# Optimization experiments

Measured on AMD Instinct MI355X. Metric: run time of the kernel, lower is better.

## Reference

```python
import jax, jax.numpy as jnp
import numpy as np

N = 100000      # nodes
E = 1600000     # edges (avg degree 16)
DIN = 128
DH = 128
DOUT = 16
G = 512         # graphs in batch


def setup_inputs() -> dict:
    key = jax.random.key(0)
    ks = jax.random.split(key, 12)
    def lin(k, fan_in, shape):
        return jax.random.uniform(k, shape, jnp.float32, -1.0, 1.0) / np.sqrt(fan_in)
    return {
        "x": jax.random.normal(ks[0], (N, DIN), jnp.float32),
        "edge_index": jax.random.randint(ks[1], (2, E), 0, N, jnp.int32),
        "edge_weight": jax.random.uniform(ks[2], (E,), jnp.float32),
        "batch": jnp.sort(jax.random.randint(ks[3], (N,), 0, G, jnp.int32)),
        "W1": lin(ks[4], DIN, (DIN, DH)), "b1": jnp.zeros((DH,), jnp.float32),
        "W2": lin(ks[5], DH, (DH, DH)),  "b2": jnp.zeros((DH,), jnp.float32),
        "W3": lin(ks[6], DH, (DH, DH)),  "b3": jnp.zeros((DH,), jnp.float32),
        "Wlin": lin(ks[7], DH, (DH, DOUT)), "blin": lin(ks[8], DH, (DOUT,)),
    }


def gcn_norm(edge_index, edge_weight, num_nodes):
    # PyG gcn_norm: add self-loops (weight 1), symmetric normalization
    loop = jnp.arange(num_nodes, dtype=edge_index.dtype)
    row = jnp.concatenate([edge_index[0], loop])
    col = jnp.concatenate([edge_index[1], loop])
    ew = jnp.concatenate([edge_weight, jnp.ones((num_nodes,), edge_weight.dtype)])
    deg = jax.ops.segment_sum(ew, col, num_segments=num_nodes)
    dinv = jnp.where(deg > 0, jax.lax.rsqrt(jnp.where(deg > 0, deg, 1.0)), 0.0)
    norm = dinv[row] * ew * dinv[col]
    return row, col, norm


def gcn_conv(x, W, b, row, col, norm, num_nodes):
    h = x @ W                                   # [N, d_out]
    msg = h[row] * norm[:, None]                # gather + scale  [E+N, d_out]
    out = jax.ops.segment_sum(msg, col, num_segments=num_nodes)
    return out + b


def reference(x, edge_index, edge_weight, batch, W1, b1, W2, b2, W3, b3, Wlin, blin):
    num_nodes = x.shape[0]
    row, col, norm = gcn_norm(edge_index, edge_weight, num_nodes)
    h = jax.nn.relu(gcn_conv(x, W1, b1, row, col, norm, num_nodes))
    h = jax.nn.relu(gcn_conv(h, W2, b2, row, col, norm, num_nodes))
    h = gcn_conv(h, W3, b3, row, col, norm, num_nodes)
    # global mean pool over graphs
    sums = jax.ops.segment_sum(h, batch, num_segments=G)          # [G, DH]
    cnt = jax.ops.segment_sum(jnp.ones((num_nodes,), h.dtype), batch, num_segments=G)
    hG = sums / jnp.maximum(cnt, 1.0)[:, None]
    # dropout is identity in eval mode
    return hG @ Wlin + blin
```

## Files before the change

### kernel.cpp

```cpp
#include <hip/hip_runtime.h>
#include <hip/hip_bf16.h>

#define NB 512
#define MAXBKT 512
#define PB 4

typedef __attribute__((ext_vector_type(8))) unsigned short ushort8;
typedef __attribute__((ext_vector_type(8))) short bf16x8;
typedef __attribute__((ext_vector_type(4))) float f32x4;

__device__ __forceinline__ unsigned short f2bf(float f) {
    unsigned u = __float_as_uint(f);
    unsigned r = (u + 0x7FFF + ((u >> 16) & 1)) >> 16;
    return (unsigned short)r;
}

__global__ __launch_bounds__(256) void k_wt3_hist(const float* __restrict__ W1,
                                                  const float* __restrict__ W2,
                                                  const float* __restrict__ W3,
                                                  const float* __restrict__ Wlin,
                                                  unsigned short* __restrict__ WT1,
                                                  unsigned short* __restrict__ WT2,
                                                  unsigned short* __restrict__ WLT,
                                                  const int* __restrict__ col, int E, int e2,
                                                  int per, int* __restrict__ cnt, int nbkt) {
    int b = blockIdx.x;
    if (b < 128) {
        const float* W = (b < 64) ? W1 : W2;
        unsigned short* WT = (b < 64) ? WT1 : WT2;
        int idx = (b & 63) * 256 + threadIdx.x;
        int nn = idx >> 7, k = idx & 127;
        WT[nn * 128 + k] = f2bf(W[k * 128 + nn]);
        return;
    }
    if (b < 136) {
        int idx = (b - 128) * 256 + threadIdx.x;
        int c = idx >> 7, k = idx & 127;
        float s = 0.f;
        for (int j = 0; j < 128; ++j) s += W3[k * 128 + j] * Wlin[j * 16 + c];
        WLT[c * 128 + k] = f2bf(s);
        return;
    }
    int hb = b - 136;
    __shared__ int h[MAXBKT];
    int t = threadIdx.x;
    for (int i = t; i < nbkt; i += 256) h[i] = 0;
    __syncthreads();
    int s = hb * per, e = min(s + per, e2);
    for (int i = s + t; i < e; i += 256) {
        int dst = (i < E) ? col[i] : i - E;
        atomicAdd(&h[dst >> 8], 1);
    }
    __syncthreads();
    for (int i = t; i < nbkt; i += 256) cnt[i * NB + hb] = h[i];
}

#define SCAN_T 256
#define SCAN_E 1024

__global__ void k_scan_a(const int* __restrict__ cnt, int n,
                         int* __restrict__ outp, int* __restrict__ bsum) {
    __shared__ int s[SCAN_T];
    int t = threadIdx.x, b = blockIdx.x;
    int base = b * SCAN_E + t * 4;
    int c0 = (base + 0 < n) ? cnt[base + 0] : 0;
    int c1 = (base + 1 < n) ? cnt[base + 1] : 0;
    int c2 = (base + 2 < n) ? cnt[base + 2] : 0;
    int c3 = (base + 3 < n) ? cnt[base + 3] : 0;
    int tsum = c0 + c1 + c2 + c3;
    s[t] = tsum; __syncthreads();
    for (int off = 1; off < SCAN_T; off <<= 1) {
        int v = (t >= off) ? s[t - off] : 0;
        __syncthreads();
        s[t] += v;
        __syncthreads();
    }
    int excl = s[t] - tsum;
    if (base + 0 < n) outp[base + 0] = excl;
    if (base + 1 < n) outp[base + 1] = excl + c0;
    if (base + 2 < n) outp[base + 2] = excl + c0 + c1;
    if (base + 3 < n) outp[base + 3] = excl + c0 + c1 + c2;
    if (t == 0) bsum[b] = s[SCAN_T - 1];
}

__global__ __launch_bounds__(256) void k_scan_b(int* __restrict__ bsum, int nb) {
    __shared__ int s[256];
    int t = threadIdx.x;
    int v = (t < nb) ? bsum[t] : 0;
    s[t] = v; __syncthreads();
    for (int off = 1; off < 256; off <<= 1) {
        int u = (t >= off) ? s[t - off] : 0;
        __syncthreads();
        s[t] += u;
        __syncthreads();
    }
    if (t < nb) bsum[t] = s[t] - v;
}

__global__ __launch_bounds__(256) void k_scatter1(const int* __restrict__ row,
                                                  const int* __restrict__ col,
                                                  const float* __restrict__ ew,
                                                  int E, int e2, int per,
                                                  const int* __restrict__ S,
                                                  const int* __restrict__ bsum,
                                                  uint2* __restrict__ csrR, int nbkt) {
    __shared__ int cur[MAXBKT];
    int t = threadIdx.x;
    for (int i = t; i < nbkt; i += 256) {
        int idx = i * NB + blockIdx.x;
        cur[i] = S[idx] + bsum[idx >> 10];
    }
    __syncthreads();
    int s = blockIdx.x * per, e = min(s + per, e2);
    for (int i = s + t; i < e; i += 256) {
        int src, dst; float w;
        if (i < E) { src = row[i]; dst = col[i]; w = ew[i]; }
        else       { src = dst = i - E; w = 1.0f; }
        int slot = atomicAdd(&cur[dst >> 8], 1);
        csrR[slot] = make_uint2(((unsigned)src << 8) | (unsigned)(dst & 255),
                                __float_as_uint(w));
    }
}

__global__ __launch_bounds__(256) void k_build(const uint2* __restrict__ csrR,
                                               const int* __restrict__ S,
                                               const int* __restrict__ bsum,
                                               int n, int e2,
                                               float2* __restrict__ csrF,
                                               float* __restrict__ dinv,
                                               int* __restrict__ rowptr, int nbkt) {
    __shared__ int   cnt[256];
    __shared__ float wsm[256];
    __shared__ int   off[256];
    __shared__ float dvs[256];
    __shared__ int   curs[256];
    int b = blockIdx.x, t = threadIdx.x;
    cnt[t] = 0; wsm[t] = 0.f;
    __syncthreads();
    int i0 = b * NB;
    int base = S[i0] + bsum[i0 >> 10];
    int end;
    if (b + 1 < nbkt) { int i1 = (b + 1) * NB; end = S[i1] + bsum[i1 >> 10]; }
    else end = e2;
    for (int i = base + t; i < end; i += 256) {
        uint2 r = csrR[i];
        int d = r.x & 255;
        atomicAdd(&cnt[d], 1);
        atomicAdd(&wsm[d], __uint_as_float(r.y));
    }
    __syncthreads();
    int   myc = cnt[t];
    float w   = wsm[t];
    float dv  = (w > 0.f) ? rsqrtf(w) : 0.f;
    dvs[t] = dv;
    off[t] = myc;
    __syncthreads();
    for (int o = 1; o < 256; o <<= 1) {
        int v = (t >= o) ? off[t - o] : 0;
        __syncthreads();
        off[t] += v;
        __syncthreads();
    }
    int excl = off[t] - myc;
    int node = b * 256 + t;
    if (node < n) { dinv[node] = dv; rowptr[node] = base + excl; }
    if (b == nbkt - 1 && t == 0) rowptr[n] = e2;
    curs[t] = excl;
    __syncthreads();
    for (int i = base + t; i < end; i += 256) {
        uint2 r = csrR[i];
        int d = r.x & 255;
        int src = (int)(r.x >> 8);
        int p = base + atomicAdd(&curs[d], 1);
        csrF[p] = make_float2(__int_as_float(src), __uint_as_float(r.y) * dvs[d]);
    }
}

template<typename T>
__global__ __launch_bounds__(256) void k_gemm_mfma(const T* __restrict__ H,
                                                   const unsigned short* __restrict__ WT,
                                                   const float* __restrict__ dinv,
                                                   unsigned short* __restrict__ O, int n) {
    int wv = threadIdx.x >> 6, lane = threadIdx.x & 63;
    int rowBase = blockIdx.x * 64 + wv * 16;
    int lr = lane & 15;
    int lk = (lane >> 4) * 8;

    int arow = min(rowBase + lr, n - 1);
    bf16x8 a[4];
#pragma unroll
    for (int kk = 0; kk < 4; ++kk) {
        if constexpr (sizeof(T) == 4) {
            const float4* p = (const float4*)&H[(size_t)arow * 128 + kk * 32 + lk];
            float4 h0 = p[0], h1 = p[1];
            bf16x8 av;
            av[0] = (short)f2bf(h0.x); av[1] = (short)f2bf(h0.y);
            av[2] = (short)f2bf(h0.z); av[3] = (short)f2bf(h0.w);
            av[4] = (short)f2bf(h1.x); av[5] = (short)f2bf(h1.y);
            av[6] = (short)f2bf(h1.z); av[7] = (short)f2bf(h1.w);
            a[kk] = av;
        } else {
            a[kk] = *(const bf16x8*)&H[(size_t)arow * 128 + kk * 32 + lk];
        }
    }

    f32x4 acc[8] = {};
#pragma unroll
    for (int c = 0; c < 8; ++c) {
#pragma unroll
        for (int kk = 0; kk < 4; ++kk) {
            bf16x8 b = *(const bf16x8*)&WT[(size_t)(c * 16 + lr) * 128 + kk * 32 + lk];
            acc[c] = __builtin_amdgcn_mfma_f32_16x16x32_bf16(a[kk], b, acc[c], 0, 0, 0);
        }
    }

#pragma unroll
    for (int r = 0; r < 4; ++r) {
        int node = rowBase + (lane >> 4) * 4 + r;
        if (node < n) {
            float sc = dinv[node];
#pragma unroll
            for (int c = 0; c < 8; ++c)
                O[(size_t)node * 128 + c * 16 + lr] = f2bf(acc[c][r] * sc);
        }
    }
}

__global__ __launch_bounds__(256) void k_gemmP(const unsigned short* __restrict__ H,
                                               const unsigned short* __restrict__ WLT,
                                               const float* __restrict__ dinv,
                                               float* __restrict__ P, int n) {
    int wv = threadIdx.x >> 6, lane = threadIdx.x & 63;
    int rowBase = blockIdx.x * 64 + wv * 16;
    int lr = lane & 15;
    int lk = (lane >> 4) * 8;

    int arow = min(rowBase + lr, n - 1);
    f32x4 acc = {};
#pragma unroll
    for (int kk = 0; kk < 4; ++kk) {
        bf16x8 a = *(const bf16x8*)&H[(size_t)arow * 128 + kk * 32 + lk];
        bf16x8 b = *(const bf16x8*)&WLT[(size_t)lr * 128 + kk * 32 + lk];
        acc = __builtin_amdgcn_mfma_f32_16x16x32_bf16(a, b, acc, 0, 0, 0);
    }
#pragma unroll
    for (int r = 0; r < 4; ++r) {
        int node = rowBase + (lane >> 4) * 4 + r;
        if (node < n) P[(size_t)node * 16 + lr] = acc[r] * dinv[node];
    }
}

template<bool RELU>
__global__ __launch_bounds__(256) void k_agg(const uint4* __restrict__ Hw,
                                             const int* __restrict__ rowptr,
                                             const float2* __restrict__ csr,
                                             const float* __restrict__ bias,
                                             unsigned short* __restrict__ out, int n) {
    int wv = threadIdx.x >> 6, lane = threadIdx.x & 63;
    int g = lane >> 4, sl = lane & 15;
    int node = blockIdx.x * 16 + wv * 4 + g;
    bool act = node < n;
    int s = 0, e = 0;
    if (act) { s = rowptr[node]; e = rowptr[node + 1]; }
    float a0 = 0.f, a1 = 0.f, a2 = 0.f, a3 = 0.f, a4 = 0.f, a5 = 0.f, a6 = 0.f, a7 = 0.f;

#define FMA8(V, W8) do {                                              \
    float _w = (W8);                                                  \
    a0 += __uint_as_float((V).x << 16) * _w;                          \
    a1 += __uint_as_float((V).x & 0xFFFF0000u) * _w;                  \
    a2 += __uint_as_float((V).y << 16) * _w;                          \
    a3 += __uint_as_float((V).y & 0xFFFF0000u) * _w;                  \
    a4 += __uint_as_float((V).z << 16) * _w;                          \
    a5 += __uint_as_float((V).z & 0xFFFF0000u) * _w;                  \
    a6 += __uint_as_float((V).w << 16) * _w;                          \
    a7 += __uint_as_float((V).w & 0xFFFF0000u) * _w;                  \
} while (0)

    int i = s;
    for (; i + 2 <= e; i += 2) {
        float2 p0 = csr[i], p1 = csr[i + 1];
        uint4 v0 = Hw[(size_t)__float_as_int(p0.x) * 16 + sl];
        uint4 v1 = Hw[(size_t)__float_as_int(p1.x) * 16 + sl];
        FMA8(v0, p0.y); FMA8(v1, p1.y);
    }
    if (i < e) {
        float2 pp = csr[i];
        uint4 v = Hw[(size_t)__float_as_int(pp.x) * 16 + sl];
        FMA8(v, pp.y);
    }
#undef FMA8

    if (act) {
        const float4* b4 = (const float4*)&bias[sl * 8];
        float4 b0 = b4[0], b1 = b4[1];
        a0 += b0.x; a1 += b0.y; a2 += b0.z; a3 += b0.w;
        a4 += b1.x; a5 += b1.y; a6 += b1.z; a7 += b1.w;
        if (RELU) {
            a0 = fmaxf(a0, 0.f); a1 = fmaxf(a1, 0.f); a2 = fmaxf(a2, 0.f); a3 = fmaxf(a3, 0.f);
            a4 = fmaxf(a4, 0.f); a5 = fmaxf(a5, 0.f); a6 = fmaxf(a6, 0.f); a7 = fmaxf(a7, 0.f);
        }
        ushort8 o;
        o[0] = f2bf(a0); o[1] = f2bf(a1); o[2] = f2bf(a2); o[3] = f2bf(a3);
        o[4] = f2bf(a4); o[5] = f2bf(a5); o[6] = f2bf(a6); o[7] = f2bf(a7);
        *(ushort8*)&out[(size_t)node * 128 + sl * 8] = o;
    }
}

__device__ __forceinline__ int lower_bound_i(const int* a, int n, int key) {
    int lo = 0, hi = n;
    while (lo < hi) { int mid = (lo + hi) >> 1; if (a[mid] < key) lo = mid + 1; else hi = mid; }
    return lo;
}

__global__ __launch_bounds__(256) void k_agg_pool(const float4* __restrict__ P4,
                                                  const int* __restrict__ rowptr,
                                                  const float2* __restrict__ csr,
                                                  const int* __restrict__ batch,
                                                  int n, float* __restrict__ partial) {
    int g = blockIdx.x >> 2, part = blockIdx.x & (PB - 1);
    int start = lower_bound_i(batch, n, g);
    int end   = lower_bound_i(batch, n, g + 1);
    int cn = end - start;
    int ns = start + (cn * part) / PB;
    int ne = start + (cn * (part + 1)) / PB;
    int es = rowptr[ns], ee = rowptr[ne];
    int t = threadIdx.x, grp = t >> 2, sl4 = t & 3;
    float a0 = 0.f, a1 = 0.f, a2 = 0.f, a3 = 0.f;
    int i = es + grp;
    for (; i + 64 < ee; i += 128) {
        float2 p0 = csr[i], p1 = csr[i + 64];
        float4 v0 = P4[(size_t)__float_as_int(p0.x) * 4 + sl4];
        float4 v1 = P4[(size_t)__float_as_int(p1.x) * 4 + sl4];
        a0 += v0.x * p0.y; a1 += v0.y * p0.y; a2 += v0.z * p0.y; a3 += v0.w * p0.y;
        a0 += v1.x * p1.y; a1 += v1.y * p1.y; a2 += v1.z * p1.y; a3 += v1.w * p1.y;
    }
    if (i < ee) {
        float2 pp = csr[i];
        float4 v = P4[(size_t)__float_as_int(pp.x) * 4 + sl4];
        a0 += v.x * pp.y; a1 += v.y * pp.y; a2 += v.z * pp.y; a3 += v.w * pp.y;
    }
    __shared__ float red[64][20];
    *(float4*)&red[grp][sl4 * 4] = make_float4(a0, a1, a2, a3);
    __syncthreads();
    if (t < 16) {
        float s = 0.f;
        for (int k2 = 0; k2 < 64; ++k2) s += red[k2][t];
        partial[(size_t)blockIdx.x * 16 + t] = s;
    }
}

__global__ void k_poolfin(const float* __restrict__ partial, const int* __restrict__ batch,
                          const float* __restrict__ b3, const float* __restrict__ Wlin,
                          const float* __restrict__ blin, float* __restrict__ out, int n) {
    int g = blockIdx.x, t = threadIdx.x;
    if (t >= 16) return;
    int start = lower_bound_i(batch, n, g);
    int end   = lower_bound_i(batch, n, g + 1);
    int cn = end - start;
    float s = partial[(size_t)(g * PB + 0) * 16 + t] + partial[(size_t)(g * PB + 1) * 16 + t]
            + partial[(size_t)(g * PB + 2) * 16 + t] + partial[(size_t)(g * PB + 3) * 16 + t];
    float bw = 0.f;
    for (int ch = 0; ch < 128; ++ch) bw += b3[ch] * Wlin[ch * 16 + t];
    out[g * 16 + t] = (cn > 0) ? s / (float)cn + bw + blin[t] : blin[t];
}

extern "C" void kernel_launch(void* const* d_in, const int* in_sizes, int n_in,
                              void* d_out, int out_size, void* d_ws, size_t ws_size,
                              hipStream_t stream) {
    const float* x    = (const float*)d_in[0];
    const int*   ei   = (const int*)d_in[1];
    const float* ew   = (const float*)d_in[2];
    const int*   batch= (const int*)d_in[3];
    const float* W1   = (const float*)d_in[4];
    const float* b1   = (const float*)d_in[5];
    const float* W2   = (const float*)d_in[6];
    const float* b2   = (const float*)d_in[7];
    const float* W3   = (const float*)d_in[8];
    const float* b3   = (const float*)d_in[9];
    const float* Wlin = (const float*)d_in[10];
    const float* blin = (const float*)d_in[11];
    float* out = (float*)d_out;

    int n  = in_sizes[0] / 128;
    int E  = in_sizes[2];
    int e2 = E + n;
    int G  = out_size / 16;
    const int* row = ei;
    const int* col = ei + E;

    int nbkt = (n + 255) >> 8;
    int M    = nbkt * NB;

    char* ws = (char*)d_ws;
    size_t off = 0;
    auto alloc = [&](size_t bytes) -> void* {
        void* p = ws + off;
        off = (off + bytes + 255) & ~255UL;
        return p;
    };
    size_t rawBytes = (size_t)e2 * 8;
    size_t hBytes   = (size_t)n * 128 * 2;
    void* regionA = alloc(rawBytes > hBytes ? rawBytes : hBytes);
    uint2*  csrR  = (uint2*)regionA;
    unsigned short* bufH = (unsigned short*)regionA;
    unsigned short* bufHw = (unsigned short*)alloc((size_t)n * 128 * 2);
    float2* csrF  = (float2*)alloc((size_t)e2 * 8);
    int*    cntA  = (int*)  alloc((size_t)M * 4);
    int*    S     = (int*)  alloc((size_t)M * 4);
    int*    bsum  = (int*)  alloc(4096);
    float*  dinv  = (float*)alloc((size_t)n * 4);
    int*    rowptr= (int*)  alloc((size_t)(n + 1) * 4);
    unsigned short* WT1 = (unsigned short*)alloc(128 * 128 * 2);
    unsigned short* WT2 = (unsigned short*)alloc(128 * 128 * 2);
    unsigned short* WLT = (unsigned short*)alloc(16 * 128 * 2);
    float*  P       = (float*)alloc((size_t)n * 16 * 4);
    float*  partial = (float*)alloc((size_t)G * PB * 16 * 4);
    (void)ws_size;

    int per = (e2 + NB - 1) / NB;
    int nbScan = (M + SCAN_E - 1) / SCAN_E;

    k_wt3_hist<<<136 + NB, 256, 0, stream>>>(W1, W2, W3, Wlin, WT1, WT2, WLT,
                                             col, E, e2, per, cntA, nbkt);
    k_scan_a<<<nbScan, SCAN_T, 0, stream>>>(cntA, M, S, bsum);
    k_scan_b<<<1, 256, 0, stream>>>(bsum, nbScan);
    k_scatter1<<<NB, 256, 0, stream>>>(row, col, ew, E, e2, per, S, bsum, csrR, nbkt);
    k_build<<<nbkt, 256, 0, stream>>>(csrR, S, bsum, n, e2, csrF, dinv, rowptr, nbkt);

    int gb = (n + 63) / 64;
    int ab = (n + 15) / 16;
    k_gemm_mfma<float><<<gb, 256, 0, stream>>>(x, WT1, dinv, bufHw, n);
    k_agg<true><<<ab, 256, 0, stream>>>((const uint4*)bufHw, rowptr, csrF, b1, bufH, n);
    k_gemm_mfma<unsigned short><<<gb, 256, 0, stream>>>(bufH, WT2, dinv, bufHw, n);
    k_agg<true><<<ab, 256, 0, stream>>>((const uint4*)bufHw, rowptr, csrF, b2, bufH, n);
    k_gemmP<<<gb, 256, 0, stream>>>(bufH, WLT, dinv, P, n);
    k_agg_pool<<<G * PB, 256, 0, stream>>>((const float4*)P, rowptr, csrF, batch, n, partial);
    k_poolfin<<<G, 64, 0, stream>>>(partial, batch, b3, Wlin, blin, out, n);
}
```

Before: 301.0 us.

## Fuse neighbor aggregation with the following layer's GEMM via LDS staging

Each aggregation kernel now writes its 16 aggregated, bias-added, ReLU'd bf16 rows to shared memory and immediately multiplies them by the next layer's weight matrix with MFMA. The intermediate hidden tensor is no longer written to and re-read from global memory, and two kernel launches are removed. Each block of 16 nodes splits the 8 output column tiles across 4 waves. The cost is re-reading the weight matrix from L2 per 16-node block, and the projection variant uses only one wave for its GEMM. It also adds a block-wide barrier after the gather phase.

```diff
diff --git a/kernel.cpp b/kernel.cpp
--- a/kernel.cpp
+++ b/kernel.cpp
@@ -176,8 +176,7 @@
     }
 }
 
-template<typename T>
-__global__ __launch_bounds__(256) void k_gemm_mfma(const T* __restrict__ H,
+__global__ __launch_bounds__(256) void k_gemm_mfma(const float* __restrict__ H,
                                                    const unsigned short* __restrict__ WT,
                                                    const float* __restrict__ dinv,
                                                    unsigned short* __restrict__ O, int n) {
@@ -190,18 +189,14 @@
     bf16x8 a[4];
 #pragma unroll
     for (int kk = 0; kk < 4; ++kk) {
-        if constexpr (sizeof(T) == 4) {
-            const float4* p = (const float4*)&H[(size_t)arow * 128 + kk * 32 + lk];
-            float4 h0 = p[0], h1 = p[1];
-            bf16x8 av;
-            av[0] = (short)f2bf(h0.x); av[1] = (short)f2bf(h0.y);
-            av[2] = (short)f2bf(h0.z); av[3] = (short)f2bf(h0.w);
-            av[4] = (short)f2bf(h1.x); av[5] = (short)f2bf(h1.y);
-            av[6] = (short)f2bf(h1.z); av[7] = (short)f2bf(h1.w);
-            a[kk] = av;
-        } else {
-            a[kk] = *(const bf16x8*)&H[(size_t)arow * 128 + kk * 32 + lk];
-        }
+        const float4* p = (const float4*)&H[(size_t)arow * 128 + kk * 32 + lk];
+        float4 h0 = p[0], h1 = p[1];
+        bf16x8 av;
+        av[0] = (short)f2bf(h0.x); av[1] = (short)f2bf(h0.y);
+        av[2] = (short)f2bf(h0.z); av[3] = (short)f2bf(h0.w);
+        av[4] = (short)f2bf(h1.x); av[5] = (short)f2bf(h1.y);
+        av[6] = (short)f2bf(h1.z); av[7] = (short)f2bf(h1.w);
+        a[kk] = av;
     }
 
     f32x4 acc[8] = {};
@@ -226,43 +221,38 @@
     }
 }
 
-__global__ __launch_bounds__(256) void k_gemmP(const unsigned short* __restrict__ H,
-                                               const unsigned short* __restrict__ WLT,
-                                               const float* __restrict__ dinv,
-                                               float* __restrict__ P, int n) {
-    int wv = threadIdx.x >> 6, lane = threadIdx.x & 63;
-    int rowBase = blockIdx.x * 64 + wv * 16;
-    int lr = lane & 15;
-    int lk = (lane >> 4) * 8;
-
-    int arow = min(rowBase + lr, n - 1);
-    f32x4 acc = {};
-#pragma unroll
-    for (int kk = 0; kk < 4; ++kk) {
-        bf16x8 a = *(const bf16x8*)&H[(size_t)arow * 128 + kk * 32 + lk];
-        bf16x8 b = *(const bf16x8*)&WLT[(size_t)lr * 128 + kk * 32 + lk];
-        acc = __builtin_amdgcn_mfma_f32_16x16x32_bf16(a, b, acc, 0, 0, 0);
-    }
-#pragma unroll
-    for (int r = 0; r < 4; ++r) {
-        int node = rowBase + (lane >> 4) * 4 + r;
-        if (node < n) P[(size_t)node * 16 + lr] = acc[r] * dinv[node];
-    }
-}
-
-template<bool RELU>
-__global__ __launch_bounds__(256) void k_agg(const uint4* __restrict__ Hw,
-                                             const int* __restrict__ rowptr,
-                                             const float2* __restrict__ csr,
-                                             const float* __restrict__ bias,
-                                             unsigned short* __restrict__ out, int n) {
-    int wv = threadIdx.x >> 6, lane = threadIdx.x & 63;
-    int g = lane >> 4, sl = lane & 15;
-    int node = blockIdx.x * 16 + wv * 4 + g;
-    bool act = node < n;
-    int s = 0, e = 0;
-    if (act) { s = rowptr[node]; e = rowptr[node + 1]; }
-    float a0 = 0.f, a1 = 0.f, a2 = 0.f, a3 = 0.f, a4 = 0.f, a5 = 0.f, a6 = 0.f, a7 = 0.f;
+#define AGG_BODY(BIAS)                                                          \
+    int t = threadIdx.x;                                                        \
+    int wv = t >> 6, lane = t & 63;                                             \
+    int g = lane >> 4, sl = lane & 15;                                          \
+    int node = blockIdx.x * 16 + wv * 4 + g;                                    \
+    int s = 0, e = 0;                                                           \
+    if (node < n) { s = rowptr[node]; e = rowptr[node + 1]; }                   \
+    float a0 = 0.f, a1 = 0.f, a2 = 0.f, a3 = 0.f,                               \
+          a4 = 0.f, a5 = 0.f, a6 = 0.f, a7 = 0.f;                               \
+    int i = s;                                                                  \
+    for (; i + 2 <= e; i += 2) {                                                \
+        float2 p0 = csr[i], p1 = csr[i + 1];                                    \
+        uint4 v0 = Hw[(size_t)__float_as_int(p0.x) * 16 + sl];                  \
+        uint4 v1 = Hw[(size_t)__float_as_int(p1.x) * 16 + sl];                  \
+        FMA8(v0, p0.y); FMA8(v1, p1.y);                                         \
+    }                                                                           \
+    if (i < e) {                                                                \
+        float2 pp = csr[i];                                                     \
+        uint4 v = Hw[(size_t)__float_as_int(pp.x) * 16 + sl];                   \
+        FMA8(v, pp.y);                                                          \
+    }                                                                           \
+    const float4* b4 = (const float4*)&(BIAS)[sl * 8];                          \
+    float4 bb0 = b4[0], bb1 = b4[1];                                            \
+    a0 = fmaxf(a0 + bb0.x, 0.f); a1 = fmaxf(a1 + bb0.y, 0.f);                   \
+    a2 = fmaxf(a2 + bb0.z, 0.f); a3 = fmaxf(a3 + bb0.w, 0.f);                   \
+    a4 = fmaxf(a4 + bb1.x, 0.f); a5 = fmaxf(a5 + bb1.y, 0.f);                   \
+    a6 = fmaxf(a6 + bb1.z, 0.f); a7 = fmaxf(a7 + bb1.w, 0.f);                   \
+    ushort8 o;                                                                  \
+    o[0] = f2bf(a0); o[1] = f2bf(a1); o[2] = f2bf(a2); o[3] = f2bf(a3);         \
+    o[4] = f2bf(a4); o[5] = f2bf(a5); o[6] = f2bf(a6); o[7] = f2bf(a7);         \
+    *(ushort8*)&lds[wv * 4 + g][sl * 8] = o;                                    \
+    __syncthreads();
 
 #define FMA8(V, W8) do {                                              \
     float _w = (W8);                                                  \
@@ -276,35 +266,70 @@
     a7 += __uint_as_float((V).w & 0xFFFF0000u) * _w;                  \
 } while (0)
 
-    int i = s;
-    for (; i + 2 <= e; i += 2) {
-        float2 p0 = csr[i], p1 = csr[i + 1];
-        uint4 v0 = Hw[(size_t)__float_as_int(p0.x) * 16 + sl];
-        uint4 v1 = Hw[(size_t)__float_as_int(p1.x) * 16 + sl];
-        FMA8(v0, p0.y); FMA8(v1, p1.y);
-    }
-    if (i < e) {
-        float2 pp = csr[i];
-        uint4 v = Hw[(size_t)__float_as_int(pp.x) * 16 + sl];
-        FMA8(v, pp.y);
-    }
+__global__ __launch_bounds__(256) void k_agg_gemm(const uint4* __restrict__ Hw,
+                                                  const int* __restrict__ rowptr,
+                                                  const float2* __restrict__ csr,
+                                                  const float* __restrict__ bias,
+                                                  const unsigned short* __restrict__ WT,
+                                                  const float* __restrict__ dinv,
+                                                  unsigned short* __restrict__ O, int n) {
+    __shared__ __align__(16) unsigned short lds[16][132];
+    AGG_BODY(bias)
+    int lr = lane & 15;
+    int lk = (lane >> 4) * 8;
+    bf16x8 a[4];
+#pragma unroll
+    for (int kk = 0; kk < 4; ++kk)
+        a[kk] = *(const bf16x8*)&lds[lr][kk * 32 + lk];
+    f32x4 acc[2] = {};
+#pragma unroll
+    for (int c2 = 0; c2 < 2; ++c2) {
+        int c = wv * 2 + c2;
+#pragma unroll
+        for (int kk = 0; kk < 4; ++kk) {
+            bf16x8 b = *(const bf16x8*)&WT[(size_t)(c * 16 + lr) * 128 + kk * 32 + lk];
+            acc[c2] = __builtin_amdgcn_mfma_f32_16x16x32_bf16(a[kk], b, acc[c2], 0, 0, 0);
+        }
+    }
+#pragma unroll
+    for (int r = 0; r < 4; ++r) {
+        int n2 = blockIdx.x * 16 + (lane >> 4) * 4 + r;
+        if (n2 < n) {
+            float sc = dinv[n2];
+            O[(size_t)n2 * 128 + (wv * 2 + 0) * 16 + lr] = f2bf(acc[0][r] * sc);
+            O[(size_t)n2 * 128 + (wv * 2 + 1) * 16 + lr] = f2bf(acc[1][r] * sc);
+        }
+    }
+}
+
+__global__ __launch_bounds__(256) void k_agg_gemmP(const uint4* __restrict__ Hw,
+                                                   const int* __restrict__ rowptr,
+                                                   const float2* __restrict__ csr,
+                                                   const float* __restrict__ bias,
+                                                   const unsigned short* __restrict__ WLT,
+                                                   const float* __restrict__ dinv,
+                                                   float* __restrict__ P, int n) {
+    __shared__ __align__(16) unsigned short lds[16][132];
+    AGG_BODY(bias)
+    if (wv == 0) {
+        int lr = lane & 15;
+        int lk = (lane >> 4) * 8;
+        f32x4 acc = {};
+#pragma unroll
+        for (int kk = 0; kk < 4; ++kk) {
+            bf16x8 a = *(const bf16x8*)&lds[lr][kk * 32 + lk];
+            bf16x8 b = *(const bf16x8*)&WLT[(size_t)lr * 128 + kk * 32 + lk];
+            acc = __builtin_amdgcn_mfma_f32_16x16x32_bf16(a, b, acc, 0, 0, 0);
+        }
+#pragma unroll
+        for (int r = 0; r < 4; ++r) {
+            int n2 = blockIdx.x * 16 + (lane >> 4) * 4 + r;
+            if (n2 < n) P[(size_t)n2 * 16 + lr] = acc[r] * dinv[n2];
+        }
+    }
+}
 #undef FMA8
-
-    if (act) {
-        const float4* b4 = (const float4*)&bias[sl * 8];
-        float4 b0 = b4[0], b1 = b4[1];
-        a0 += b0.x; a1 += b0.y; a2 += b0.z; a3 += b0.w;
-        a4 += b1.x; a5 += b1.y; a6 += b1.z; a7 += b1.w;
-        if (RELU) {
-            a0 = fmaxf(a0, 0.f); a1 = fmaxf(a1, 0.f); a2 = fmaxf(a2, 0.f); a3 = fmaxf(a3, 0.f);
-            a4 = fmaxf(a4, 0.f); a5 = fmaxf(a5, 0.f); a6 = fmaxf(a6, 0.f); a7 = fmaxf(a7, 0.f);
-        }
-        ushort8 o;
-        o[0] = f2bf(a0); o[1] = f2bf(a1); o[2] = f2bf(a2); o[3] = f2bf(a3);
-        o[4] = f2bf(a4); o[5] = f2bf(a5); o[6] = f2bf(a6); o[7] = f2bf(a7);
-        *(ushort8*)&out[(size_t)node * 128 + sl * 8] = o;
-    }
-}
+#undef AGG_BODY
 
 __device__ __forceinline__ int lower_bound_i(const int* a, int n, int key) {
     int lo = 0, hi = n;
@@ -402,8 +427,8 @@
     size_t hBytes   = (size_t)n * 128 * 2;
     void* regionA = alloc(rawBytes > hBytes ? rawBytes : hBytes);
     uint2*  csrR  = (uint2*)regionA;
-    unsigned short* bufH = (unsigned short*)regionA;
-    unsigned short* bufHw = (unsigned short*)alloc((size_t)n * 128 * 2);
+    unsigned short* bufM2 = (unsigned short*)regionA;
+    unsigned short* bufM1 = (unsigned short*)alloc((size_t)n * 128 * 2);
     float2* csrF  = (float2*)alloc((size_t)e2 * 8);
     int*    cntA  = (int*)  alloc((size_t)M * 4);
     int*    S     = (int*)  alloc((size_t)M * 4);
@@ -429,11 +454,9 @@
 
     int gb = (n + 63) / 64;
     int ab = (n + 15) / 16;
-    k_gemm_mfma<float><<<gb, 256, 0, stream>>>(x, WT1, dinv, bufHw, n);
-    k_agg<true><<<ab, 256, 0, stream>>>((const uint4*)bufHw, rowptr, csrF, b1, bufH, n);
-    k_gemm_mfma<unsigned short><<<gb, 256, 0, stream>>>(bufH, WT2, dinv, bufHw, n);
-    k_agg<true><<<ab, 256, 0, stream>>>((const uint4*)bufHw, rowptr, csrF, b2, bufH, n);
-    k_gemmP<<<gb, 256, 0, stream>>>(bufH, WLT, dinv, P, n);
+    k_gemm_mfma<<<gb, 256, 0, stream>>>(x, WT1, dinv, bufM1, n);
+    k_agg_gemm<<<ab, 256, 0, stream>>>((const uint4*)bufM1, rowptr, csrF, b1, WT2, dinv, bufM2, n);
+    k_agg_gemmP<<<ab, 256, 0, stream>>>((const uint4*)bufM2, rowptr, csrF, b2, WLT, dinv, P, n);
     k_agg_pool<<<G * PB, 256, 0, stream>>>((const float4*)P, rowptr, csrF, batch, n, partial);
     k_poolfin<<<G, 64, 0, stream>>>(partial, batch, b3, Wlin, blin, out, n);
 }
```

Result: faster. 279.5 us (median of 2 runs) (-7.1%).

## Shard feature columns into 16-wide slabs for cache-local aggregation

Applied to the files above, without the earlier changes.

The GEMM now writes its output in a column-sharded layout (8 slabs of n×16 bf16). A new aggregation kernel runs each shard in its own blocks (shard = blockIdx&7), so every block gathers only from a 3.2 MB slab instead of the full 25.6 MB feature matrix. The aim is to improve L2/MALL hit rates for the random neighbour gathers. In exchange, each gather becomes an 8-byte ushort4 load instead of 16 bytes, and the CSR index and weight stream is re-read once per shard (8×).

```diff
diff --git a/kernel.cpp b/kernel.cpp
--- a/kernel.cpp
+++ b/kernel.cpp
@@ -13,6 +13,9 @@
     unsigned u = __float_as_uint(f);
     unsigned r = (u + 0x7FFF + ((u >> 16) & 1)) >> 16;
     return (unsigned short)r;
+}
+__device__ __forceinline__ float bf2f(unsigned short u) {
+    return __uint_as_float((unsigned)u << 16);
 }
 
 __global__ __launch_bounds__(256) void k_wt3_hist(const float* __restrict__ W1,
@@ -221,9 +224,48 @@
             float sc = dinv[node];
 #pragma unroll
             for (int c = 0; c < 8; ++c)
-                O[(size_t)node * 128 + c * 16 + lr] = f2bf(acc[c][r] * sc);
+                O[((size_t)c * n + node) * 16 + lr] = f2bf(acc[c][r] * sc);
         }
     }
+}
+
+__global__ __launch_bounds__(256) void k_agg_sh(const unsigned short* __restrict__ Hw,
+                                                const int* __restrict__ rowptr,
+                                                const float2* __restrict__ csr,
+                                                const float* __restrict__ bias,
+                                                unsigned short* __restrict__ h, int n) {
+    int shard = blockIdx.x & 7;
+    int grp   = blockIdx.x >> 3;
+    int t = threadIdx.x;
+    int wv = t >> 6, lane = t & 63;
+    int nq = lane >> 2, cl = lane & 3;
+    int node = grp * 64 + wv * 16 + nq;
+    if (node >= n) return;
+    int s = rowptr[node], e = rowptr[node + 1];
+    const unsigned short* base = Hw + (size_t)shard * n * 16;
+    float a0 = 0.f, a1 = 0.f, a2 = 0.f, a3 = 0.f;
+    int i = s;
+    for (; i + 2 <= e; i += 2) {
+        float2 p0 = csr[i], p1 = csr[i + 1];
+        ushort4 v0 = *(const ushort4*)&base[(size_t)__float_as_int(p0.x) * 16 + cl * 4];
+        ushort4 v1 = *(const ushort4*)&base[(size_t)__float_as_int(p1.x) * 16 + cl * 4];
+        a0 += bf2f(v0.x) * p0.y; a1 += bf2f(v0.y) * p0.y;
+        a2 += bf2f(v0.z) * p0.y; a3 += bf2f(v0.w) * p0.y;
+        a0 += bf2f(v1.x) * p1.y; a1 += bf2f(v1.y) * p1.y;
+        a2 += bf2f(v1.z) * p1.y; a3 += bf2f(v1.w) * p1.y;
+    }
+    if (i < e) {
+        float2 pp = csr[i];
+        ushort4 v = *(const ushort4*)&base[(size_t)__float_as_int(pp.x) * 16 + cl * 4];
+        a0 += bf2f(v.x) * pp.y; a1 += bf2f(v.y) * pp.y;
+        a2 += bf2f(v.z) * pp.y; a3 += bf2f(v.w) * pp.y;
+    }
+    float4 bb = *(const float4*)&bias[shard * 16 + cl * 4];
+    a0 = fmaxf(a0 + bb.x, 0.f); a1 = fmaxf(a1 + bb.y, 0.f);
+    a2 = fmaxf(a2 + bb.z, 0.f); a3 = fmaxf(a3 + bb.w, 0.f);
+    ushort4 o;
+    o.x = f2bf(a0); o.y = f2bf(a1); o.z = f2bf(a2); o.w = f2bf(a3);
+    *(ushort4*)&h[(size_t)node * 128 + shard * 16 + cl * 4] = o;
 }
 
 __global__ __launch_bounds__(256) void k_gemmP(const unsigned short* __restrict__ H,
@@ -247,62 +289,6 @@
     for (int r = 0; r < 4; ++r) {
         int node = rowBase + (lane >> 4) * 4 + r;
         if (node < n) P[(size_t)node * 16 + lr] = acc[r] * dinv[node];
-    }
-}
-
-template<bool RELU>
-__global__ __launch_bounds__(256) void k_agg(const uint4* __restrict__ Hw,
-                                             const int* __restrict__ rowptr,
-                                             const float2* __restrict__ csr,
-                                             const float* __restrict__ bias,
-                                             unsigned short* __restrict__ out, int n) {
-    int wv = threadIdx.x >> 6, lane = threadIdx.x & 63;
-    int g = lane >> 4, sl = lane & 15;
-    int node = blockIdx.x * 16 + wv * 4 + g;
-    bool act = node < n;
-    int s = 0, e = 0;
-    if (act) { s = rowptr[node]; e = rowptr[node + 1]; }
-    float a0 = 0.f, a1 = 0.f, a2 = 0.f, a3 = 0.f, a4 = 0.f, a5 = 0.f, a6 = 0.f, a7 = 0.f;
-
-#define FMA8(V, W8) do {                                              \
-    float _w = (W8);                                                  \
-    a0 += __uint_as_float((V).x << 16) * _w;                          \
-    a1 += __uint_as_float((V).x & 0xFFFF0000u) * _w;                  \
-    a2 += __uint_as_float((V).y << 16) * _w;                          \
-    a3 += __uint_as_float((V).y & 0xFFFF0000u) * _w;                  \
-    a4 += __uint_as_float((V).z << 16) * _w;                          \
-    a5 += __uint_as_float((V).z & 0xFFFF0000u) * _w;                  \
-    a6 += __uint_as_float((V).w << 16) * _w;                          \
-    a7 += __uint_as_float((V).w & 0xFFFF0000u) * _w;                  \
-} while (0)
-
-    int i = s;
-    for (; i + 2 <= e; i += 2) {
-        float2 p0 = csr[i], p1 = csr[i + 1];
-        uint4 v0 = Hw[(size_t)__float_as_int(p0.x) * 16 + sl];
-        uint4 v1 = Hw[(size_t)__float_as_int(p1.x) * 16 + sl];
-        FMA8(v0, p0.y); FMA8(v1, p1.y);
-    }
-    if (i < e) {
-        float2 pp = csr[i];
-        uint4 v = Hw[(size_t)__float_as_int(pp.x) * 16 + sl];
-        FMA8(v, pp.y);
-    }
-#undef FMA8
-
-    if (act) {
-        const float4* b4 = (const float4*)&bias[sl * 8];
-        float4 b0 = b4[0], b1 = b4[1];
-        a0 += b0.x; a1 += b0.y; a2 += b0.z; a3 += b0.w;
-        a4 += b1.x; a5 += b1.y; a6 += b1.z; a7 += b1.w;
-        if (RELU) {
-            a0 = fmaxf(a0, 0.f); a1 = fmaxf(a1, 0.f); a2 = fmaxf(a2, 0.f); a3 = fmaxf(a3, 0.f);
-            a4 = fmaxf(a4, 0.f); a5 = fmaxf(a5, 0.f); a6 = fmaxf(a6, 0.f); a7 = fmaxf(a7, 0.f);
-        }
-        ushort8 o;
-        o[0] = f2bf(a0); o[1] = f2bf(a1); o[2] = f2bf(a2); o[3] = f2bf(a3);
-        o[4] = f2bf(a4); o[5] = f2bf(a5); o[6] = f2bf(a6); o[7] = f2bf(a7);
-        *(ushort8*)&out[(size_t)node * 128 + sl * 8] = o;
     }
 }
 
@@ -402,8 +388,8 @@
     size_t hBytes   = (size_t)n * 128 * 2;
     void* regionA = alloc(rawBytes > hBytes ? rawBytes : hBytes);
     uint2*  csrR  = (uint2*)regionA;
-    unsigned short* bufH = (unsigned short*)regionA;
-    unsigned short* bufHw = (unsigned short*)alloc((size_t)n * 128 * 2);
+    unsigned short* bufX = (unsigned short*)regionA;
+    unsigned short* bufY = (unsigned short*)alloc((size_t)n * 128 * 2);
     float2* csrF  = (float2*)alloc((size_t)e2 * 8);
     int*    cntA  = (int*)  alloc((size_t)M * 4);
     int*    S     = (int*)  alloc((size_t)M * 4);
@@ -428,12 +414,11 @@
     k_build<<<nbkt, 256, 0, stream>>>(csrR, S, bsum, n, e2, csrF, dinv, rowptr, nbkt);
 
     int gb = (n + 63) / 64;
-    int ab = (n + 15) / 16;
-    k_gemm_mfma<float><<<gb, 256, 0, stream>>>(x, WT1, dinv, bufHw, n);
-    k_agg<true><<<ab, 256, 0, stream>>>((const uint4*)bufHw, rowptr, csrF, b1, bufH, n);
-    k_gemm_mfma<unsigned short><<<gb, 256, 0, stream>>>(bufH, WT2, dinv, bufHw, n);
-    k_agg<true><<<ab, 256, 0, stream>>>((const uint4*)bufHw, rowptr, csrF, b2, bufH, n);
-    k_gemmP<<<gb, 256, 0, stream>>>(bufH, WLT, dinv, P, n);
+    k_gemm_mfma<float><<<gb, 256, 0, stream>>>(x, WT1, dinv, bufX, n);
+    k_agg_sh<<<8 * gb, 256, 0, stream>>>(bufX, rowptr, csrF, b1, bufY, n);
+    k_gemm_mfma<unsigned short><<<gb, 256, 0, stream>>>(bufY, WT2, dinv, bufX, n);
+    k_agg_sh<<<8 * gb, 256, 0, stream>>>(bufX, rowptr, csrF, b2, bufY, n);
+    k_gemmP<<<gb, 256, 0, stream>>>(bufY, WLT, dinv, P, n);
     k_agg_pool<<<G * PB, 256, 0, stream>>>((const float4*)P, rowptr, csrF, batch, n, partial);
     k_poolfin<<<G, 64, 0, stream>>>(partial, batch, b3, Wlin, blin, out, n);
 }
```

Result: slower. 415.6 us (+38.1%).
